# Kernel optimization log

Measured on AMD Instinct MI355X. Metric: run time of the kernel, lower is better.

Reference implementation:

```python
import jax, jax.numpy as jnp
import numpy as np

EPS = 1e-5
KS = [3, 3]   # kernel_sizes from get_ksd(5)
DS = [1, 2]   # dilates from get_ksd(5)


def bn_relu(t, g, b, m, v):
    # inference-mode BatchNorm2d followed by ReLU; per-channel params over axis 1
    scale = (g / jnp.sqrt(v + EPS))[None, :, None, None]
    shift = (b - m * g / jnp.sqrt(v + EPS))[None, :, None, None]
    return jax.nn.relu(t * scale + shift)


def dw_conv(t, w, r, p):
    # depthwise conv, kernel k, dilation r, padding p (same spatial size)
    C = t.shape[1]
    return jax.lax.conv_general_dilated(
        t, w, window_strides=(1, 1), padding=((p, p), (p, p)),
        rhs_dilation=(r, r), dimension_numbers=('NCHW', 'OIHW', 'NCHW'),
        feature_group_count=C)


def unfold(t, k, r, p):
    # torch nn.Unfold(kernel_size=k, dilation=r, padding=p) reshaped to [N,C,k*k,H,W]
    N, C, H, W = t.shape
    tp = jnp.pad(t, ((0, 0), (0, 0), (p, p), (p, p)))
    patches = [tp[:, :, i * r:i * r + H, j * r:j * r + W]
               for i in range(k) for j in range(k)]
    return jnp.stack(patches, axis=2)  # [N, C, k*k, H, W]


def branch(y, x, k, r, dw_w, bg, bb, bm, bv, pw_w, pw_b):
    p = (r * (k - 1) + 1) // 2
    t = bn_relu(dw_conv(y, dw_w, r, p), bg, bb, bm, bv)        # [N, yC, H, W]
    kern = jnp.einsum('nchw,oc->nohw', t, pw_w) + pw_b[None, :, None, None]
    N, C, H, W = x.shape
    kern = kern.reshape(N, C, k * k, H, W)                     # per-pixel kernels
    ux = unfold(x, k, r, p)                                    # [N, C, k*k, H, W]
    return (ux * kern).sum(axis=2)                             # [N, C, H, W]


def setup_inputs() -> dict:
    key = jax.random.key(0)
    ks = jax.random.split(key, 24)
    N, C, H, W = 4, 64, 160, 160
    d = {
        'y': jax.random.normal(ks[0], (N, C, H, W), jnp.float32),
        'x': jax.random.normal(ks[1], (N, C, H, W), jnp.float32),
    }
    i = 2
    for b, k in enumerate(KS):
        d[f'dw_w{b}'] = jax.random.normal(ks[i], (C, 1, k, k), jnp.float32) * 0.3; i += 1
        d[f'bn_g{b}'] = jax.random.uniform(ks[i], (C,), jnp.float32, 0.5, 1.5); i += 1
        d[f'bn_b{b}'] = jax.random.normal(ks[i], (C,), jnp.float32) * 0.1; i += 1
        d[f'bn_m{b}'] = jax.random.normal(ks[i], (C,), jnp.float32) * 0.1; i += 1
        d[f'bn_v{b}'] = jax.random.uniform(ks[i], (C,), jnp.float32, 0.5, 1.5); i += 1
        d[f'pw_w{b}'] = jax.random.normal(ks[i], (C * k * k, C), jnp.float32) * (1.0 / np.sqrt(C)); i += 1
        d[f'pw_b{b}'] = jax.random.normal(ks[i], (C * k * k,), jnp.float32) * 0.05; i += 1
    d['norm_g'] = jax.random.uniform(ks[i], (C,), jnp.float32, 0.5, 1.5); i += 1
    d['norm_b'] = jax.random.normal(ks[i], (C,), jnp.float32) * 0.1; i += 1
    d['norm_m'] = jax.random.normal(ks[i], (C,), jnp.float32) * 0.1; i += 1
    d['norm_v'] = jax.random.uniform(ks[i], (C,), jnp.float32, 0.5, 1.5)
    return d


def reference(y, x,
              dw_w0, bn_g0, bn_b0, bn_m0, bn_v0, pw_w0, pw_b0,
              dw_w1, bn_g1, bn_b1, bn_m1, bn_v1, pw_w1, pw_b1,
              norm_g, norm_b, norm_m, norm_v):
    combined = branch(y, x, KS[0], DS[0], dw_w0, bn_g0, bn_b0, bn_m0, bn_v0, pw_w0, pw_b0)
    combined = combined + branch(y, x, KS[1], DS[1], dw_w1, bn_g1, bn_b1, bn_m1, bn_v1, pw_w1, pw_b1)
    return bn_relu(combined, norm_g, norm_b, norm_m, norm_v)
```

## Files before the change

### kernel.cpp

```cpp
#include <hip/hip_runtime.h>

#define HH 160
#define WW 160

typedef __attribute__((ext_vector_type(8))) short bf16x8;
typedef __attribute__((ext_vector_type(4))) float f32x4;

static __device__ __forceinline__ unsigned short f32_to_bf16_rne(float f) {
    unsigned u = __float_as_uint(f);
    unsigned r = (u + 0x7FFFu + ((u >> 16) & 1u)) >> 16;
    return (unsigned short)r;
}
static __device__ __forceinline__ float bf16_to_f32(unsigned short h) {
    return __uint_as_float(((unsigned)h) << 16);
}

static __device__ __forceinline__ void stage16(const char* g, char* lbase, int lane) {
#if __has_builtin(__builtin_amdgcn_global_load_lds)
    __builtin_amdgcn_global_load_lds(
        (const __attribute__((address_space(1))) unsigned int*)g,
        (__attribute__((address_space(3))) unsigned int*)lbase, 16, 0, 0);
#else
    *(f32x4*)(lbase + lane * 16) = *(const f32x4*)g;
#endif
}

__global__ __launch_bounds__(256) void prep_w_kernel(const float* __restrict__ pw0,
                                                     const float* __restrict__ pw1,
                                                     unsigned short* __restrict__ wF) {
    int idx = blockIdx.x * 256 + threadIdx.x;
    if (idx >= 18432) return;
    int lane = idx & 63;
    int frag = idx >> 6;
    int comp = frag & 1;
    int kh   = (frag >> 1) & 1;
    int ct   = (frag >> 2) & 3;
    int t    = frag >> 4;
    int bb   = t / 9;
    int kk   = t - bb * 9;
    const float* pw = bb ? pw1 : pw0;
    int c = ct * 16 + (lane & 15);
    bf16x8 pack;
    #pragma unroll
    for (int j = 0; j < 8; ++j) {
        int cp = kh * 32 + (lane >> 4) * 8 + j;
        float v = pw[(c * 9 + kk) * 64 + cp];
        unsigned short hb = f32_to_bf16_rne(v);
        if (comp == 0) pack[j] = (short)hb;
        else           pack[j] = (short)f32_to_bf16_rne(v - bf16_to_f32(hb));
    }
    *(bf16x8*)&wF[frag * 512 + lane * 8] = pack;
}

__global__ __launch_bounds__(256, 2) void fused_kernel(
    const float* __restrict__ y,   const float* __restrict__ x,
    const float* __restrict__ dw0, const float* __restrict__ g0,
    const float* __restrict__ bb0, const float* __restrict__ m0,
    const float* __restrict__ v0,  const float* __restrict__ pwb0,
    const float* __restrict__ dw1, const float* __restrict__ g1,
    const float* __restrict__ bb1, const float* __restrict__ m1,
    const float* __restrict__ v1,  const float* __restrict__ pwb1,
    const float* __restrict__ ng,  const float* __restrict__ nbb,
    const float* __restrict__ nm,  const float* __restrict__ nv,
    const unsigned short* __restrict__ wF, float* __restrict__ out)
{
    __shared__ unsigned short t_hi[128 * 64];
    __shared__ unsigned short t_lo[128 * 64];
    __shared__ __align__(16) char bbuf[2 * 16384];
    __shared__ float dwl[2 * 576];
    __shared__ float pwbl[2 * 576];
    __shared__ float scb[2 * 64], shb[2 * 64], nscl[64], nshl[64];

    const int tid  = threadIdx.x;
    const int lane = tid & 63;
    const int wid  = tid >> 6;
    const int cl   = lane & 15;
    const int pg   = lane >> 4;

    const int bid0 = blockIdx.x;
    const int bid  = (bid0 & 7) * 100 + (bid0 >> 3);
    const int n    = bid / 200;
    const int rem  = bid - n * 200;
    const int ht   = rem / 5;
    const int wt   = rem - ht * 5;
    const int h    = ht * 4;
    const int w0   = wt * 32;

    const float* ybase = y + (size_t)n * (64 * HH * WW);
    const float* xbase = x + (size_t)n * (64 * HH * WW);
    const char*  wfb8  = (const char*)wF;
    char*        bb    = bbuf;

    for (int e = tid; e < 576; e += 256) {
        dwl[e] = dw0[e];  dwl[576 + e] = dw1[e];
        pwbl[e] = pwb0[e]; pwbl[576 + e] = pwb1[e];
    }
    if (tid < 64) {
        float s0 = g0[tid] * rsqrtf(v0[tid] + 1e-5f);
        scb[tid] = s0;      shb[tid] = bb0[tid] - m0[tid] * s0;
        float s1 = g1[tid] * rsqrtf(v1[tid] + 1e-5f);
        scb[64 + tid] = s1; shb[64 + tid] = bb1[tid] - m1[tid] * s1;
        float sn = ng[tid] * rsqrtf(nv[tid] + 1e-5f);
        nscl[tid] = sn;     nshl[tid] = nbb[tid] - nm[tid] * sn;
    }
    #pragma unroll
    for (int it = 0; it < 4; ++it)
        stage16(wfb8 + ((wid + it * 4) << 10) + lane * 16,
                bb + ((wid + it * 4) << 10), lane);
    __syncthreads();

    float outacc[2][4][4];
    #pragma unroll
    for (int mt = 0; mt < 2; ++mt)
        #pragma unroll
        for (int ct = 0; ct < 4; ++ct)
            #pragma unroll
            for (int rr = 0; rr < 4; ++rr) outacc[mt][ct][rr] = 0.f;

    #pragma unroll
    for (int b = 0; b < 2; ++b) {
        const int r = b + 1;
        if (b) __syncthreads();

        {
            const int px = tid & 127;
            const int rl = px >> 5, wl = px & 31;
            const int cb = (tid >> 7) * 4;
            #pragma unroll 1
            for (int it = 0; it < 4; ++it) {
                const int chunk = cb + it;
                const int cp0 = chunk * 8;
                bf16x8 h8, l8;
                #pragma unroll
                for (int jc = 0; jc < 8; ++jc) {
                    const int cp = cp0 + jc;
                    float a = 0.f;
                    #pragma unroll
                    for (int i = 0; i < 3; ++i) {
                        const int hr = h + rl + (i - 1) * r;
                        const bool hok = (unsigned)hr < (unsigned)HH;
                        const float* yr = ybase + ((size_t)cp * HH + hr) * WW;
                        #pragma unroll
                        for (int j = 0; j < 3; ++j) {
                            const int wc = w0 + wl + (j - 1) * r;
                            float yv = (hok && (unsigned)wc < (unsigned)WW) ? yr[wc] : 0.f;
                            a = fmaf(yv, dwl[b * 576 + cp * 9 + i * 3 + j], a);
                        }
                    }
                    float tv = fmaxf(fmaf(a, scb[b * 64 + cp], shb[b * 64 + cp]), 0.f);
                    unsigned short hb = f32_to_bf16_rne(tv);
                    h8[jc] = (short)hb;
                    l8[jc] = (short)f32_to_bf16_rne(tv - bf16_to_f32(hb));
                }
                const int phys = chunk ^ ((px >> 1) & 7);
                *(bf16x8*)&t_hi[px * 64 + phys * 8] = h8;
                *(bf16x8*)&t_lo[px * 64 + phys * 8] = l8;
            }
        }
        __syncthreads();

        bf16x8 afr0[2][2], afr1[2][2];
        #pragma unroll
        for (int kh = 0; kh < 2; ++kh) {
            {
                const int px = wid * 32 + cl;
                const int phys = (kh * 4 + pg) ^ ((px >> 1) & 7);
                afr0[kh][0] = *(const bf16x8*)&t_hi[px * 64 + phys * 8];
                afr0[kh][1] = *(const bf16x8*)&t_lo[px * 64 + phys * 8];
            }
            {
                const int px = wid * 32 + 16 + cl;
                const int phys = (kh * 4 + pg) ^ ((px >> 1) & 7);
                afr1[kh][0] = *(const bf16x8*)&t_hi[px * 64 + phys * 8];
                afr1[kh][1] = *(const bf16x8*)&t_lo[px * 64 + phys * 8];
            }
        }

        #pragma unroll 1
        for (int di = 0; di < 3; ++di) {
            const int xrow = h + wid + (di - 1) * r;
            const bool rowok = (unsigned)xrow < (unsigned)HH;

            float win[4][2][12];
            #pragma unroll
            for (int ct = 0; ct < 4; ++ct) {
                const int c = ct * 16 + cl;
                const float* xrp = xbase + ((size_t)c * HH + xrow) * WW;
                #pragma unroll
                for (int mt = 0; mt < 2; ++mt) {
                    const int pgb = w0 + mt * 16 + pg * 4;
                    #pragma unroll
                    for (int q = 0; q < 3; ++q) {
                        const int col = pgb - 4 + q * 4;
                        f32x4 v = {0.f, 0.f, 0.f, 0.f};
                        if (rowok && col >= 0 && col <= (WW - 4))
                            v = *(const f32x4*)(xrp + col);
                        win[ct][mt][q * 4 + 0] = v[0];
                        win[ct][mt][q * 4 + 1] = v[1];
                        win[ct][mt][q * 4 + 2] = v[2];
                        win[ct][mt][q * 4 + 3] = v[3];
                    }
                }
            }

            #pragma unroll
            for (int dj = 0; dj < 3; ++dj) {
                const int kk  = 3 * di + dj;
                const int tn  = b * 9 + kk;
                const int par = tn & 1;
                const char* bcur = bb + (par << 14);
                char*       bnxt = bb + ((par ^ 1) << 14);

                if (tn < 17) {
                    const char* s = wfb8 + ((size_t)(tn + 1) << 14);
                    #pragma unroll
                    for (int it = 0; it < 4; ++it)
                        stage16(s + ((wid + it * 4) << 10) + lane * 16,
                                bnxt + ((wid + it * 4) << 10), lane);
                }

                #pragma unroll
                for (int ct = 0; ct < 4; ++ct) {
                    bf16x8 bfr[2][2];
                    #pragma unroll
                    for (int kh = 0; kh < 2; ++kh)
                        #pragma unroll
                        for (int cm = 0; cm < 2; ++cm)
                            bfr[kh][cm] = *(const bf16x8*)(bcur +
                                ((ct * 4 + kh * 2 + cm) << 10) + lane * 16);

                    const int c = ct * 16 + cl;
                    const float bv = pwbl[b * 576 + c * 9 + kk];
                    f32x4 k0 = {bv, bv, bv, bv};
                    f32x4 k1 = k0;
                    #pragma unroll
                    for (int p = 0; p < 3; ++p) {
                        const int ac = (p == 2) ? 1 : 0;
                        const int bc = (p == 1) ? 1 : 0;
                        #pragma unroll
                        for (int kh = 0; kh < 2; ++kh) {
                            k0 = __builtin_amdgcn_mfma_f32_16x16x32_bf16(
                                afr0[kh][ac], bfr[kh][bc], k0, 0, 0, 0);
                            k1 = __builtin_amdgcn_mfma_f32_16x16x32_bf16(
                                afr1[kh][ac], bfr[kh][bc], k1, 0, 0, 0);
                        }
                    }
                    #pragma unroll
                    for (int rr = 0; rr < 4; ++rr) {
                        outacc[0][ct][rr] = fmaf(k0[rr], win[ct][0][4 + (dj - 1) * r + rr],
                                                 outacc[0][ct][rr]);
                        outacc[1][ct][rr] = fmaf(k1[rr], win[ct][1][4 + (dj - 1) * r + rr],
                                                 outacc[1][ct][rr]);
                    }
                }
                __syncthreads();
            }
        }
    }

    {
        const int hrow = h + wid;
        #pragma unroll
        for (int mt = 0; mt < 2; ++mt) {
            const int wc0 = w0 + mt * 16 + pg * 4;
            #pragma unroll
            for (int ct = 0; ct < 4; ++ct) {
                const int c = ct * 16 + cl;
                const float sn = nscl[c], sh = nshl[c];
                f32x4 o;
                #pragma unroll
                for (int rr = 0; rr < 4; ++rr)
                    o[rr] = fmaxf(fmaf(outacc[mt][ct][rr], sn, sh), 0.f);
                *(f32x4*)&out[(((size_t)n * 64 + c) * HH + hrow) * WW + wc0] = o;
            }
        }
    }
}

extern "C" void kernel_launch(void* const* d_in, const int* in_sizes, int n_in,
                              void* d_out, int out_size, void* d_ws, size_t ws_size,
                              hipStream_t stream) {
    const float* y    = (const float*)d_in[0];
    const float* x    = (const float*)d_in[1];
    const float* dw0  = (const float*)d_in[2];
    const float* g0   = (const float*)d_in[3];
    const float* b0   = (const float*)d_in[4];
    const float* m0   = (const float*)d_in[5];
    const float* v0   = (const float*)d_in[6];
    const float* pw0  = (const float*)d_in[7];
    const float* pwb0 = (const float*)d_in[8];
    const float* dw1  = (const float*)d_in[9];
    const float* g1   = (const float*)d_in[10];
    const float* b1   = (const float*)d_in[11];
    const float* m1   = (const float*)d_in[12];
    const float* v1   = (const float*)d_in[13];
    const float* pw1  = (const float*)d_in[14];
    const float* pwb1 = (const float*)d_in[15];
    const float* ng   = (const float*)d_in[16];
    const float* nb   = (const float*)d_in[17];
    const float* nm   = (const float*)d_in[18];
    const float* nv   = (const float*)d_in[19];

    unsigned short* wF = (unsigned short*)d_ws;

    prep_w_kernel<<<72, 256, 0, stream>>>(pw0, pw1, wF);
    fused_kernel<<<800, 256, 0, stream>>>(y, x,
                                          dw0, g0, b0, m0, v0, pwb0,
                                          dw1, g1, b1, m1, v1, pwb1,
                                          ng, nb, nm, nv, wF, (float*)d_out);
}
```

Baseline: 270.2 us.

## Drop low-order bf16 split for activations, stream x loads, raise occupancy

Activations t are now kept only as a single bf16 (hi) fragment instead of a hi+lo split, so each tap needs four MFMAs instead of six and the t_lo shared buffer is gone. The BN folds move into the prep kernel and are read from global memory, per-tap x windows are loaded right where they are used instead of as a 96-float register window, and launch bounds go to 3 blocks per CU. The goal is less LDS and fewer registers for higher occupancy, plus fewer MFMAs. In exchange, dropping the lo correction lowers the precision of the t·W product, which may exceed the tolerance.

```diff
diff --git a/kernel.cpp b/kernel.cpp
--- a/kernel.cpp
+++ b/kernel.cpp
@@ -25,11 +25,31 @@
 #endif
 }
 
-__global__ __launch_bounds__(256) void prep_w_kernel(const float* __restrict__ pw0,
-                                                     const float* __restrict__ pw1,
-                                                     unsigned short* __restrict__ wF) {
+__global__ __launch_bounds__(256) void prep_w_kernel(
+    const float* __restrict__ pw0, const float* __restrict__ pw1,
+    const float* __restrict__ g0,  const float* __restrict__ bb0,
+    const float* __restrict__ m0,  const float* __restrict__ v0,
+    const float* __restrict__ g1,  const float* __restrict__ bb1,
+    const float* __restrict__ m1,  const float* __restrict__ v1,
+    const float* __restrict__ ng,  const float* __restrict__ nbb,
+    const float* __restrict__ nm,  const float* __restrict__ nv,
+    unsigned short* __restrict__ wF, float* __restrict__ wfolds) {
     int idx = blockIdx.x * 256 + threadIdx.x;
-    if (idx >= 18432) return;
+    if (idx >= 18432) {
+        if (blockIdx.x == 72 && threadIdx.x < 64) {
+            int c = threadIdx.x;
+            float s0 = g0[c] * rsqrtf(v0[c] + 1e-5f);
+            wfolds[c]        = s0;
+            wfolds[64 + c]   = bb0[c] - m0[c] * s0;
+            float s1 = g1[c] * rsqrtf(v1[c] + 1e-5f);
+            wfolds[128 + c]  = s1;
+            wfolds[192 + c]  = bb1[c] - m1[c] * s1;
+            float sn = ng[c] * rsqrtf(nv[c] + 1e-5f);
+            wfolds[256 + c]  = sn;
+            wfolds[320 + c]  = nbb[c] - nm[c] * sn;
+        }
+        return;
+    }
     int lane = idx & 63;
     int frag = idx >> 6;
     int comp = frag & 1;
@@ -52,24 +72,16 @@
     *(bf16x8*)&wF[frag * 512 + lane * 8] = pack;
 }
 
-__global__ __launch_bounds__(256, 2) void fused_kernel(
+__global__ __launch_bounds__(256, 3) void fused_kernel(
     const float* __restrict__ y,   const float* __restrict__ x,
-    const float* __restrict__ dw0, const float* __restrict__ g0,
-    const float* __restrict__ bb0, const float* __restrict__ m0,
-    const float* __restrict__ v0,  const float* __restrict__ pwb0,
-    const float* __restrict__ dw1, const float* __restrict__ g1,
-    const float* __restrict__ bb1, const float* __restrict__ m1,
-    const float* __restrict__ v1,  const float* __restrict__ pwb1,
-    const float* __restrict__ ng,  const float* __restrict__ nbb,
-    const float* __restrict__ nm,  const float* __restrict__ nv,
-    const unsigned short* __restrict__ wF, float* __restrict__ out)
+    const float* __restrict__ dw0, const float* __restrict__ dw1,
+    const float* __restrict__ pwb0,const float* __restrict__ pwb1,
+    const unsigned short* __restrict__ wF, const float* __restrict__ wfolds,
+    float* __restrict__ out)
 {
     __shared__ unsigned short t_hi[128 * 64];
-    __shared__ unsigned short t_lo[128 * 64];
     __shared__ __align__(16) char bbuf[2 * 16384];
     __shared__ float dwl[2 * 576];
-    __shared__ float pwbl[2 * 576];
-    __shared__ float scb[2 * 64], shb[2 * 64], nscl[64], nshl[64];
 
     const int tid  = threadIdx.x;
     const int lane = tid & 63;
@@ -89,24 +101,13 @@
     const float* ybase = y + (size_t)n * (64 * HH * WW);
     const float* xbase = x + (size_t)n * (64 * HH * WW);
     const char*  wfb8  = (const char*)wF;
-    char*        bb    = bbuf;
-
-    for (int e = tid; e < 576; e += 256) {
-        dwl[e] = dw0[e];  dwl[576 + e] = dw1[e];
-        pwbl[e] = pwb0[e]; pwbl[576 + e] = pwb1[e];
-    }
-    if (tid < 64) {
-        float s0 = g0[tid] * rsqrtf(v0[tid] + 1e-5f);
-        scb[tid] = s0;      shb[tid] = bb0[tid] - m0[tid] * s0;
-        float s1 = g1[tid] * rsqrtf(v1[tid] + 1e-5f);
-        scb[64 + tid] = s1; shb[64 + tid] = bb1[tid] - m1[tid] * s1;
-        float sn = ng[tid] * rsqrtf(nv[tid] + 1e-5f);
-        nscl[tid] = sn;     nshl[tid] = nbb[tid] - nm[tid] * sn;
-    }
+
+    for (int e = tid; e < 1152; e += 256)
+        dwl[e] = (e < 576) ? dw0[e] : dw1[e - 576];
     #pragma unroll
     for (int it = 0; it < 4; ++it)
         stage16(wfb8 + ((wid + it * 4) << 10) + lane * 16,
-                bb + ((wid + it * 4) << 10), lane);
+                bbuf + ((wid + it * 4) << 10), lane);
     __syncthreads();
 
     float outacc[2][4][4];
@@ -130,7 +131,7 @@
             for (int it = 0; it < 4; ++it) {
                 const int chunk = cb + it;
                 const int cp0 = chunk * 8;
-                bf16x8 h8, l8;
+                bf16x8 h8;
                 #pragma unroll
                 for (int jc = 0; jc < 8; ++jc) {
                     const int cp = cp0 + jc;
@@ -147,69 +148,45 @@
                             a = fmaf(yv, dwl[b * 576 + cp * 9 + i * 3 + j], a);
                         }
                     }
-                    float tv = fmaxf(fmaf(a, scb[b * 64 + cp], shb[b * 64 + cp]), 0.f);
-                    unsigned short hb = f32_to_bf16_rne(tv);
-                    h8[jc] = (short)hb;
-                    l8[jc] = (short)f32_to_bf16_rne(tv - bf16_to_f32(hb));
+                    const float sc = wfolds[b * 128 + cp];
+                    const float sh = wfolds[b * 128 + 64 + cp];
+                    float tv = fmaxf(fmaf(a, sc, sh), 0.f);
+                    h8[jc] = (short)f32_to_bf16_rne(tv);
                 }
                 const int phys = chunk ^ ((px >> 1) & 7);
                 *(bf16x8*)&t_hi[px * 64 + phys * 8] = h8;
-                *(bf16x8*)&t_lo[px * 64 + phys * 8] = l8;
             }
         }
         __syncthreads();
 
-        bf16x8 afr0[2][2], afr1[2][2];
+        bf16x8 afr0[2], afr1[2];
         #pragma unroll
         for (int kh = 0; kh < 2; ++kh) {
             {
                 const int px = wid * 32 + cl;
                 const int phys = (kh * 4 + pg) ^ ((px >> 1) & 7);
-                afr0[kh][0] = *(const bf16x8*)&t_hi[px * 64 + phys * 8];
-                afr0[kh][1] = *(const bf16x8*)&t_lo[px * 64 + phys * 8];
+                afr0[kh] = *(const bf16x8*)&t_hi[px * 64 + phys * 8];
             }
             {
                 const int px = wid * 32 + 16 + cl;
                 const int phys = (kh * 4 + pg) ^ ((px >> 1) & 7);
-                afr1[kh][0] = *(const bf16x8*)&t_hi[px * 64 + phys * 8];
-                afr1[kh][1] = *(const bf16x8*)&t_lo[px * 64 + phys * 8];
-            }
-        }
+                afr1[kh] = *(const bf16x8*)&t_hi[px * 64 + phys * 8];
+            }
+        }
+
+        const float* pwbg = b ? pwb1 : pwb0;
+        const int xrow_base = h + wid;
 
         #pragma unroll 1
         for (int di = 0; di < 3; ++di) {
-            const int xrow = h + wid + (di - 1) * r;
+            const int xrow = xrow_base + (di - 1) * r;
             const bool rowok = (unsigned)xrow < (unsigned)HH;
-
-            float win[4][2][12];
-            #pragma unroll
-            for (int ct = 0; ct < 4; ++ct) {
-                const int c = ct * 16 + cl;
-                const float* xrp = xbase + ((size_t)c * HH + xrow) * WW;
-                #pragma unroll
-                for (int mt = 0; mt < 2; ++mt) {
-                    const int pgb = w0 + mt * 16 + pg * 4;
-                    #pragma unroll
-                    for (int q = 0; q < 3; ++q) {
-                        const int col = pgb - 4 + q * 4;
-                        f32x4 v = {0.f, 0.f, 0.f, 0.f};
-                        if (rowok && col >= 0 && col <= (WW - 4))
-                            v = *(const f32x4*)(xrp + col);
-                        win[ct][mt][q * 4 + 0] = v[0];
-                        win[ct][mt][q * 4 + 1] = v[1];
-                        win[ct][mt][q * 4 + 2] = v[2];
-                        win[ct][mt][q * 4 + 3] = v[3];
-                    }
-                }
-            }
-
-            #pragma unroll
+            #pragma unroll 1
             for (int dj = 0; dj < 3; ++dj) {
-                const int kk  = 3 * di + dj;
-                const int tn  = b * 9 + kk;
-                const int par = tn & 1;
-                const char* bcur = bb + (par << 14);
-                char*       bnxt = bb + ((par ^ 1) << 14);
+                const int kk = di * 3 + dj;
+                const int tn = b * 9 + kk;
+                const char* bcur = bbuf + ((tn & 1) << 14);
+                char*       bnxt = bbuf + (((tn & 1) ^ 1) << 14);
 
                 if (tn < 17) {
                     const char* s = wfb8 + ((size_t)(tn + 1) << 14);
@@ -219,6 +196,7 @@
                                 bnxt + ((wid + it * 4) << 10), lane);
                 }
 
+                const int colb = w0 + pg * 4 + (dj - 1) * r;
                 #pragma unroll
                 for (int ct = 0; ct < 4; ++ct) {
                     bf16x8 bfr[2][2];
@@ -230,27 +208,46 @@
                                 ((ct * 4 + kh * 2 + cm) << 10) + lane * 16);
 
                     const int c = ct * 16 + cl;
-                    const float bv = pwbl[b * 576 + c * 9 + kk];
+                    const float bv = pwbg[c * 9 + kk];
                     f32x4 k0 = {bv, bv, bv, bv};
                     f32x4 k1 = k0;
                     #pragma unroll
-                    for (int p = 0; p < 3; ++p) {
-                        const int ac = (p == 2) ? 1 : 0;
-                        const int bc = (p == 1) ? 1 : 0;
+                    for (int kh = 0; kh < 2; ++kh) {
+                        k0 = __builtin_amdgcn_mfma_f32_16x16x32_bf16(
+                            afr0[kh], bfr[kh][0], k0, 0, 0, 0);
+                        k0 = __builtin_amdgcn_mfma_f32_16x16x32_bf16(
+                            afr0[kh], bfr[kh][1], k0, 0, 0, 0);
+                        k1 = __builtin_amdgcn_mfma_f32_16x16x32_bf16(
+                            afr1[kh], bfr[kh][0], k1, 0, 0, 0);
+                        k1 = __builtin_amdgcn_mfma_f32_16x16x32_bf16(
+                            afr1[kh], bfr[kh][1], k1, 0, 0, 0);
+                    }
+
+                    const float* xrp = xbase + ((size_t)c * HH + xrow) * WW;
+                    f32x4 xv0 = {0.f, 0.f, 0.f, 0.f}, xv1 = {0.f, 0.f, 0.f, 0.f};
+                    const int col0 = colb, col1 = colb + 16;
+                    if (rowok && col0 >= 0 && col0 <= (WW - 4)) {
+                        __builtin_memcpy(&xv0, xrp + col0, 16);
+                    } else if (rowok) {
                         #pragma unroll
-                        for (int kh = 0; kh < 2; ++kh) {
-                            k0 = __builtin_amdgcn_mfma_f32_16x16x32_bf16(
-                                afr0[kh][ac], bfr[kh][bc], k0, 0, 0, 0);
-                            k1 = __builtin_amdgcn_mfma_f32_16x16x32_bf16(
-                                afr1[kh][ac], bfr[kh][bc], k1, 0, 0, 0);
+                        for (int rr = 0; rr < 4; ++rr) {
+                            const int xc = col0 + rr;
+                            if ((unsigned)xc < (unsigned)WW) xv0[rr] = xrp[xc];
                         }
                     }
+                    if (rowok && col1 >= 0 && col1 <= (WW - 4)) {
+                        __builtin_memcpy(&xv1, xrp + col1, 16);
+                    } else if (rowok) {
+                        #pragma unroll
+                        for (int rr = 0; rr < 4; ++rr) {
+                            const int xc = col1 + rr;
+                            if ((unsigned)xc < (unsigned)WW) xv1[rr] = xrp[xc];
+                        }
+                    }
                     #pragma unroll
                     for (int rr = 0; rr < 4; ++rr) {
-                        outacc[0][ct][rr] = fmaf(k0[rr], win[ct][0][4 + (dj - 1) * r + rr],
-                                                 outacc[0][ct][rr]);
-                        outacc[1][ct][rr] = fmaf(k1[rr], win[ct][1][4 + (dj - 1) * r + rr],
-                                                 outacc[1][ct][rr]);
+                        outacc[0][ct][rr] = fmaf(k0[rr], xv0[rr], outacc[0][ct][rr]);
+                        outacc[1][ct][rr] = fmaf(k1[rr], xv1[rr], outacc[1][ct][rr]);
                     }
                 }
                 __syncthreads();
@@ -266,7 +263,7 @@
             #pragma unroll
             for (int ct = 0; ct < 4; ++ct) {
                 const int c = ct * 16 + cl;
-                const float sn = nscl[c], sh = nshl[c];
+                const float sn = wfolds[256 + c], sh = wfolds[320 + c];
                 f32x4 o;
                 #pragma unroll
                 for (int rr = 0; rr < 4; ++rr)
@@ -302,10 +299,12 @@
     const float* nv   = (const float*)d_in[19];
 
     unsigned short* wF = (unsigned short*)d_ws;
-
-    prep_w_kernel<<<72, 256, 0, stream>>>(pw0, pw1, wF);
-    fused_kernel<<<800, 256, 0, stream>>>(y, x,
-                                          dw0, g0, b0, m0, v0, pwb0,
-                                          dw1, g1, b1, m1, v1, pwb1,
-                                          ng, nb, nm, nv, wF, (float*)d_out);
-}
+    float* wfolds = (float*)((char*)d_ws + 294912);
+
+    prep_w_kernel<<<73, 256, 0, stream>>>(pw0, pw1,
+                                          g0, b0, m0, v0,
+                                          g1, b1, m1, v1,
+                                          ng, nb, nm, nv, wF, wfolds);
+    fused_kernel<<<800, 256, 0, stream>>>(y, x, dw0, dw1, pwb0, pwb1,
+                                          wF, wfolds, (float*)d_out);
+}
```

Result: slower. 400.9 us (+48.4%).
